# Kernel optimization log

Measured on AMD Instinct MI355X. Metric: run time of the kernel, lower is better.

## Reference

```python
import jax, jax.numpy as jnp
import numpy as np

N = 100000

def _gcn_norm(edge_index, n):
    # PyG GCNConv default: add self-loops, symmetric deg^-1/2 normalization
    loops = jnp.arange(n, dtype=edge_index.dtype)
    src = jnp.concatenate([edge_index[0], loops])
    dst = jnp.concatenate([edge_index[1], loops])
    deg = jax.ops.segment_sum(jnp.ones_like(dst, dtype=jnp.float32), dst, num_segments=n)
    dinv = jnp.where(deg > 0, jax.lax.rsqrt(deg), 0.0)
    norm = dinv[src] * dinv[dst]  # [E+N]
    return src, dst, norm

def _gcn_conv(h, W, b, src, dst, norm, n):
    # transform then gather-scale-scatter aggregate
    h = h @ W                                   # [N, out]
    out = jax.ops.segment_sum(norm[:, None] * h[src], dst, num_segments=n)
    return out + b

def _prelu(h, a):
    return jnp.where(h > 0, h, a * h)

def _dropout(h, u, p=0.5):
    # deterministic dropout: keep where u >= p, scale by 1/(1-p)
    return jnp.where(u >= p, h / (1.0 - p), 0.0)

def setup_inputs() -> dict:
    key = jax.random.key(0)
    ks = jax.random.split(key, 12)
    D, H1, H2, C, E = 512, 128, 16, 10, 1600000
    x = jax.random.normal(ks[0], (N, D), dtype=jnp.float32)
    edge_index = jax.random.randint(ks[1], (2, E), 0, N, dtype=jnp.int64)
    u1 = jax.random.uniform(ks[2], (N, H1), dtype=jnp.float32)
    u2 = jax.random.uniform(ks[3], (N, H2), dtype=jnp.float32)
    def glorot(k, shp):
        lim = np.sqrt(6.0 / (shp[0] + shp[1]))
        return jax.random.uniform(k, shp, dtype=jnp.float32, minval=-lim, maxval=lim)
    W1 = glorot(ks[4], (D, H1)); b1 = jnp.zeros((H1,), jnp.float32)
    W2 = glorot(ks[5], (H1, H2)); b2 = jnp.zeros((H2,), jnp.float32)
    fcW = glorot(ks[6], (H2, C)); fcb = jnp.zeros((C,), jnp.float32)
    a = jnp.float32(0.25)  # PReLU init (shared single param for both layers)
    return {"x": x, "edge_index": edge_index, "W1": W1, "b1": b1, "W2": W2,
            "b2": b2, "a": a, "fcW": fcW, "fcb": fcb, "u1": u1, "u2": u2}

def reference(x, edge_index, W1, b1, W2, b2, a, fcW, fcb, u1, u2):
    src, dst, norm = _gcn_norm(edge_index, N)
    feat1 = _dropout(_prelu(_gcn_conv(x, W1, b1, src, dst, norm, N), a), u1)
    feat2 = _dropout(_prelu(_gcn_conv(feat1, W2, b2, src, dst, norm, N), a), u2)
    logits = feat2 @ fcW + fcb
    return (feat2, logits)
```

## Files before the change

### kernel.cpp

```cpp
#include <hip/hip_runtime.h>
#include <hip/hip_bf16.h>
#include <stdint.h>

#define NN 100000
#define DIN 512
#define H1C 128
#define H2C 16
#define NCLS 10
#define NB_SCAN ((NN + 255) / 256)

typedef __attribute__((ext_vector_type(8))) short s16x8;
typedef __attribute__((ext_vector_type(4))) float f32x4;
typedef __attribute__((ext_vector_type(4))) unsigned short u16x4;
typedef __attribute__((ext_vector_type(8))) unsigned short u16x8;

static __device__ __forceinline__ unsigned short f2bf(float f) {
  __hip_bfloat16 h = __float2bfloat16(f);
  return *(unsigned short*)&h;
}
static __device__ __forceinline__ float bflo(unsigned u) {
  return __uint_as_float(u << 16);
}
static __device__ __forceinline__ float bfhi(unsigned u) {
  return __uint_as_float(u & 0xffff0000u);
}

__device__ __forceinline__ int ld_src(const int* __restrict__ ei, int f, int E, int i) {
  return f ? ei[2 * (size_t)i] : ei[i];
}
__device__ __forceinline__ int ld_dst(const int* __restrict__ ei, int f, int E, int i) {
  return f ? ei[2 * ((size_t)E + (size_t)i)] : ei[(size_t)E + (size_t)i];
}

__global__ void k_pre(const int* __restrict__ ei, int* __restrict__ flag,
                      int* __restrict__ deg,
                      const float* __restrict__ W1, unsigned short* __restrict__ Wt, int n) {
  int i = blockIdx.x * 256 + threadIdx.x;
  if (blockIdx.x == 0 && threadIdx.x < 64) {
    int v = ei[2 * threadIdx.x + 1];
    unsigned long long b = __ballot(v == 0);
    if (threadIdx.x == 0) *flag = (b == ~0ull) ? 1 : 0;
  }
  if (i < n) deg[i] = 0;
  if (i < H1C * DIN) {
    int nn = i >> 9, k = i & 511;
    Wt[i] = f2bf(W1[(size_t)k * H1C + nn]);
  }
}

__global__ void k_count(const int* __restrict__ ei, const int* __restrict__ flag,
                        int E, int* __restrict__ deg, int* __restrict__ rank) {
  int i = blockIdx.x * blockDim.x + threadIdx.x;
  if (i >= E) return;
  int f = *flag;
  rank[i] = atomicAdd(&deg[ld_dst(ei, f, E, i)], 1);
}

__global__ void k_scanA(const int* __restrict__ deg, int* __restrict__ incl,
                        int* __restrict__ bsum, float* __restrict__ dinv, int n) {
  __shared__ int s[256];
  int i = blockIdx.x * 256 + threadIdx.x;
  int v = (i < n) ? deg[i] : 0;
  if (i < n) dinv[i] = rsqrtf((float)(v + 1));
  s[threadIdx.x] = v;
  __syncthreads();
  for (int off = 1; off < 256; off <<= 1) {
    int t = (threadIdx.x >= off) ? s[threadIdx.x - off] : 0;
    __syncthreads();
    s[threadIdx.x] += t;
    __syncthreads();
  }
  if (i < n) incl[i] = s[threadIdx.x];
  if (threadIdx.x == 255) bsum[blockIdx.x] = s[255];
}

__global__ void k_scanBC(const int* __restrict__ deg, const int* __restrict__ bsum,
                         int* __restrict__ offs, int n, int E, int nb) {
  __shared__ int s[512];
  int tid = threadIdx.x;
  int v = (tid < nb) ? bsum[tid] : 0;
  s[tid] = v;
  __syncthreads();
  for (int off = 1; off < 512; off <<= 1) {
    int t = (tid >= off) ? s[tid - off] : 0;
    __syncthreads();
    s[tid] += t;
    __syncthreads();
  }
  int bid = blockIdx.x;
  int pb = (bid > 0) ? s[bid - 1] : 0;
  int i = bid * 256 + (tid & 255);
  if (tid < 256 && i < n) offs[i] = offs[i] - deg[i] + pb;
  if (bid == 0 && tid == 0) offs[n] = E;
}

#define BM 64
#define BK 64
#define LDA 72
#define LDB 72
#define NGB ((NN + BM - 1) / BM)

__global__ __launch_bounds__(256) void k_sg1(const float* __restrict__ x,
                                             const unsigned short* __restrict__ Wt,
                                             unsigned int* __restrict__ h1u, int n,
                                             const int* __restrict__ ei,
                                             const int* __restrict__ flag, int E,
                                             const int* __restrict__ offs,
                                             const int* __restrict__ rank,
                                             const float* __restrict__ dinv,
                                             uint2* __restrict__ csr_sw) {
  __shared__ unsigned short As[BM * LDA];
  __shared__ unsigned short Bs[H1C * LDB];
  int tid = threadIdx.x;

  if (blockIdx.x >= NGB) {
    int i = (blockIdx.x - NGB) * 256 + tid;
    if (i < E) {
      int f = *flag;
      int s = ld_src(ei, f, E, i), d = ld_dst(ei, f, E, i);
      int pos = offs[d] + rank[i];
      uint2 rec;
      rec.x = (unsigned)s;
      rec.y = __float_as_uint(dinv[s]);
      csr_sw[pos] = rec;
    }
    return;
  }

  int wave = tid >> 6, lane = tid & 63;
  int wm = wave >> 1, wn = wave & 1;
  int bm = blockIdx.x * BM;
  int lrow = lane & 15, lk = (lane >> 4) * 8;

  f32x4 acc[2][4];
#pragma unroll
  for (int i = 0; i < 2; i++)
#pragma unroll
    for (int j = 0; j < 4; j++) acc[i][j] = (f32x4){0.f, 0.f, 0.f, 0.f};

  float4 areg[4];
  u16x8 breg[4];

  auto loadA = [&](int k0) {
#pragma unroll
    for (int p = 0; p < 4; p++) {
      int idx = p * 256 + tid;
      int r = idx >> 4, c4 = (idx & 15) * 4;
      int row = bm + r;
      areg[p] = make_float4(0.f, 0.f, 0.f, 0.f);
      if (row < n) areg[p] = *(const float4*)(x + (size_t)row * DIN + k0 + c4);
    }
  };
  auto loadB = [&](int k0) {
#pragma unroll
    for (int p = 0; p < 4; p++) {
      int idx = p * 256 + tid;
      int r = idx >> 3, c8 = (idx & 7) * 8;
      breg[p] = *(const u16x8*)&Wt[(size_t)r * DIN + k0 + c8];
    }
  };

  loadA(0);
  loadB(0);

  for (int k0 = 0; k0 < DIN; k0 += BK) {
#pragma unroll
    for (int p = 0; p < 4; p++) {
      int idx = p * 256 + tid;
      int r = idx >> 4, c4 = (idx & 15) * 4;
      u16x4 b4;
      b4.x = f2bf(areg[p].x); b4.y = f2bf(areg[p].y);
      b4.z = f2bf(areg[p].z); b4.w = f2bf(areg[p].w);
      *(u16x4*)&As[r * LDA + c4] = b4;
      int rb = idx >> 3, c8 = (idx & 7) * 8;
      int pr = (rb & 64) + (((rb & 1) + 2 * ((rb >> 5) & 1)) << 4) + ((rb >> 1) & 15);
      *(u16x8*)&Bs[pr * LDB + c8] = breg[p];
    }
    if (k0 + BK < DIN) {
      loadA(k0 + BK);
      loadB(k0 + BK);
    }
    __syncthreads();
#pragma unroll
    for (int kk = 0; kk < 2; kk++) {
      s16x8 a[2], b[4];
#pragma unroll
      for (int mi = 0; mi < 2; mi++)
        a[mi] = *(const s16x8*)&As[(wm * 32 + mi * 16 + lrow) * LDA + kk * 32 + lk];
#pragma unroll
      for (int nj = 0; nj < 4; nj++)
        b[nj] = *(const s16x8*)&Bs[(wn * 64 + nj * 16 + lrow) * LDB + kk * 32 + lk];
#pragma unroll
      for (int mi = 0; mi < 2; mi++)
#pragma unroll
        for (int nj = 0; nj < 4; nj++)
          acc[mi][nj] = __builtin_amdgcn_mfma_f32_16x16x32_bf16(a[mi], b[nj], acc[mi][nj], 0, 0, 0);
    }
    __syncthreads();
  }
#pragma unroll
  for (int mi = 0; mi < 2; mi++) {
#pragma unroll
    for (int r = 0; r < 4; r++) {
      int row = bm + wm * 32 + mi * 16 + (lane >> 4) * 4 + r;
      if (row < n) {
        unsigned p0 = ((unsigned)f2bf(acc[mi][1][r]) << 16) | (unsigned)f2bf(acc[mi][0][r]);
        unsigned p1 = ((unsigned)f2bf(acc[mi][3][r]) << 16) | (unsigned)f2bf(acc[mi][2][r]);
        h1u[(size_t)row * 64 + wn * 32 + lrow] = p0;
        h1u[(size_t)row * 64 + wn * 32 + 16 + lrow] = p1;
      }
    }
  }
}

__global__ __launch_bounds__(256) void k_agg1(const unsigned int* __restrict__ h1u,
                                              const uint2* __restrict__ csr_sw,
                                              const int* __restrict__ offs,
                                              const float* __restrict__ dinv,
                                              const float* __restrict__ b1,
                                              const float* __restrict__ aP,
                                              const float* __restrict__ u1,
                                              unsigned int* __restrict__ f1u, int n) {
  int wid = (blockIdx.x * 256 + threadIdx.x) >> 6;
  int lane = threadIdx.x & 63;
  if (wid >= n) return;
  int d = wid;
  int beg = offs[d], end = offs[d + 1];
  unsigned gs = h1u[(size_t)d * 64 + lane];
  float ax = 0.f, ay = 0.f;
  int e = beg;
  for (; e + 7 < end; e += 8) {
    uint2 r0 = csr_sw[e],     r1 = csr_sw[e + 1], r2 = csr_sw[e + 2], r3 = csr_sw[e + 3];
    uint2 r4 = csr_sw[e + 4], r5 = csr_sw[e + 5], r6 = csr_sw[e + 6], r7 = csr_sw[e + 7];
    unsigned g0 = h1u[(size_t)r0.x * 64 + lane];
    unsigned g1 = h1u[(size_t)r1.x * 64 + lane];
    unsigned g2 = h1u[(size_t)r2.x * 64 + lane];
    unsigned g3 = h1u[(size_t)r3.x * 64 + lane];
    unsigned g4 = h1u[(size_t)r4.x * 64 + lane];
    unsigned g5 = h1u[(size_t)r5.x * 64 + lane];
    unsigned g6 = h1u[(size_t)r6.x * 64 + lane];
    unsigned g7 = h1u[(size_t)r7.x * 64 + lane];
    float w0 = __uint_as_float(r0.y), w1 = __uint_as_float(r1.y);
    float w2 = __uint_as_float(r2.y), w3 = __uint_as_float(r3.y);
    float w4 = __uint_as_float(r4.y), w5 = __uint_as_float(r5.y);
    float w6 = __uint_as_float(r6.y), w7 = __uint_as_float(r7.y);
    ax += w0 * bflo(g0); ay += w0 * bfhi(g0);
    ax += w1 * bflo(g1); ay += w1 * bfhi(g1);
    ax += w2 * bflo(g2); ay += w2 * bfhi(g2);
    ax += w3 * bflo(g3); ay += w3 * bfhi(g3);
    ax += w4 * bflo(g4); ay += w4 * bfhi(g4);
    ax += w5 * bflo(g5); ay += w5 * bfhi(g5);
    ax += w6 * bflo(g6); ay += w6 * bfhi(g6);
    ax += w7 * bflo(g7); ay += w7 * bfhi(g7);
  }
  for (; e + 3 < end; e += 4) {
    uint2 r0 = csr_sw[e], r1 = csr_sw[e + 1], r2 = csr_sw[e + 2], r3 = csr_sw[e + 3];
    unsigned g0 = h1u[(size_t)r0.x * 64 + lane];
    unsigned g1 = h1u[(size_t)r1.x * 64 + lane];
    unsigned g2 = h1u[(size_t)r2.x * 64 + lane];
    unsigned g3 = h1u[(size_t)r3.x * 64 + lane];
    float w0 = __uint_as_float(r0.y), w1 = __uint_as_float(r1.y);
    float w2 = __uint_as_float(r2.y), w3 = __uint_as_float(r3.y);
    ax += w0 * bflo(g0); ay += w0 * bfhi(g0);
    ax += w1 * bflo(g1); ay += w1 * bfhi(g1);
    ax += w2 * bflo(g2); ay += w2 * bfhi(g2);
    ax += w3 * bflo(g3); ay += w3 * bfhi(g3);
  }
  for (; e < end; e++) {
    uint2 rr = csr_sw[e];
    float w = __uint_as_float(rr.y);
    unsigned g = h1u[(size_t)rr.x * 64 + lane];
    ax += w * bflo(g); ay += w * bfhi(g);
  }
  float di = dinv[d];
  ax = (ax + di * bflo(gs)) * di;
  ay = (ay + di * bfhi(gs)) * di;
  float2 bb = ((const float2*)b1)[lane];
  ax += bb.x; ay += bb.y;
  float al = *aP;
  ax = ax > 0.f ? ax : al * ax;
  ay = ay > 0.f ? ay : al * ay;
  float2 uu = ((const float2*)u1)[(size_t)d * 64 + lane];
  ax = (uu.x >= 0.5f) ? ax * 2.f : 0.f;
  ay = (uu.y >= 0.5f) ? ay * 2.f : 0.f;
  unsigned pk = ((unsigned)f2bf(ay) << 16) | (unsigned)f2bf(ax);
  f1u[(size_t)d * 64 + lane] = pk;
}

__global__ __launch_bounds__(256) void k_gemm2(const unsigned int* __restrict__ f1u,
                                               const float* __restrict__ W2,
                                               unsigned int* __restrict__ h2u, int n) {
  __shared__ float ws[H1C][H2C];
  __shared__ unsigned int fs[16][66];
  int tid = threadIdx.x;
#pragma unroll
  for (int p = 0; p < 8; p++) {
    int idx = tid + p * 256;
    ws[idx >> 4][idx & 15] = W2[idx];
  }
  int r0 = blockIdx.x * 16;
  {
    int r = tid >> 4, c4 = (tid & 15) * 4;
    int row = r0 + r;
    uint4 v = make_uint4(0, 0, 0, 0);
    if (row < n) v = *(const uint4*)(f1u + (size_t)row * 64 + c4);
    *(uint4*)&fs[r][c4] = v;
  }
  __syncthreads();
  int col = tid & 15, r = tid >> 4;
  float acc = 0.f;
#pragma unroll
  for (int k = 0; k < 64; k++) {
    unsigned u = fs[r][k];
    acc += bflo(u) * ws[2 * k][col] + bfhi(u) * ws[2 * k + 1][col];
  }
  int row = r0 + r;
  float accN = __shfl_xor(acc, 1, 64);
  if ((col & 1) == 0 && row < n) {
    unsigned pk = ((unsigned)f2bf(accN) << 16) | (unsigned)f2bf(acc);
    h2u[(size_t)row * 8 + (col >> 1)] = pk;
  }
}

__global__ __launch_bounds__(256) void k_agg2(const unsigned int* __restrict__ h2u,
                                              const uint2* __restrict__ csr_sw,
                                              const int* __restrict__ offs,
                                              const float* __restrict__ dinv,
                                              const float* __restrict__ b2,
                                              const float* __restrict__ aP,
                                              const float* __restrict__ u2,
                                              const float* __restrict__ fcW,
                                              const float* __restrict__ fcb,
                                              float* __restrict__ out_feat2,
                                              float* __restrict__ out_logits, int n) {
  int wid = (blockIdx.x * 256 + threadIdx.x) >> 6;
  int lane = threadIdx.x & 63;
  if (wid >= n) return;
  int d = wid;
  int g = lane >> 3, j = lane & 7;
  int beg = offs[d], end = offs[d + 1];
  unsigned gs = h2u[(size_t)d * 8 + j];
  float aa = 0.f, ab = 0.f;
  int e = beg + g;
  for (; e + 8 < end; e += 16) {
    uint2 r0 = csr_sw[e], r1 = csr_sw[e + 8];
    unsigned g0 = h2u[(size_t)r0.x * 8 + j];
    unsigned g1 = h2u[(size_t)r1.x * 8 + j];
    float w0 = __uint_as_float(r0.y), w1 = __uint_as_float(r1.y);
    aa += w0 * bflo(g0) + w1 * bflo(g1);
    ab += w0 * bfhi(g0) + w1 * bfhi(g1);
  }
  for (; e < end; e += 8) {
    uint2 rr = csr_sw[e];
    unsigned gg = h2u[(size_t)rr.x * 8 + j];
    float w = __uint_as_float(rr.y);
    aa += w * bflo(gg); ab += w * bfhi(gg);
  }
  aa += __shfl_xor(aa, 8, 64); aa += __shfl_xor(aa, 16, 64); aa += __shfl_xor(aa, 32, 64);
  ab += __shfl_xor(ab, 8, 64); ab += __shfl_xor(ab, 16, 64); ab += __shfl_xor(ab, 32, 64);
  float di = dinv[d];
  aa = (aa + di * bflo(gs)) * di;
  ab = (ab + di * bfhi(gs)) * di;
  aa += b2[2 * j]; ab += b2[2 * j + 1];
  float al = *aP;
  aa = aa > 0.f ? aa : al * aa;
  ab = ab > 0.f ? ab : al * ab;
  float2 uu = ((const float2*)(u2 + (size_t)d * H2C))[j];
  aa = (uu.x >= 0.5f) ? aa * 2.f : 0.f;
  ab = (uu.y >= 0.5f) ? ab * 2.f : 0.f;
  if (lane < 8) {
    float2 o; o.x = aa; o.y = ab;
    ((float2*)(out_feat2 + (size_t)d * H2C))[j] = o;
  }
  int c = lane & 15;
  int cc = (c < NCLS) ? c : 0;
  float lg = fcb[cc];
#pragma unroll
  for (int k = 0; k < 8; k++) {
    float va = __shfl(aa, k, 64);
    float vb = __shfl(ab, k, 64);
    lg += va * fcW[(2 * k) * NCLS + cc] + vb * fcW[(2 * k + 1) * NCLS + cc];
  }
  if (lane < NCLS) out_logits[(size_t)d * NCLS + c] = lg;
}

extern "C" void kernel_launch(void* const* d_in, const int* in_sizes, int n_in,
                              void* d_out, int out_size, void* d_ws, size_t ws_size,
                              hipStream_t stream) {
  const float* x   = (const float*)d_in[0];
  const int*   ei  = (const int*)d_in[1];
  const float* W1  = (const float*)d_in[2];
  const float* b1  = (const float*)d_in[3];
  const float* W2  = (const float*)d_in[4];
  const float* b2  = (const float*)d_in[5];
  const float* aP  = (const float*)d_in[6];
  const float* fcW = (const float*)d_in[7];
  const float* fcb = (const float*)d_in[8];
  const float* u1  = (const float*)d_in[9];
  const float* u2  = (const float*)d_in[10];
  const int E = in_sizes[1] / 2;

  float* out_feat2  = (float*)d_out;
  float* out_logits = (float*)d_out + (size_t)NN * H2C;

  char* w = (char*)d_ws;
  size_t off = 0;
  auto A = [&](size_t bytes) -> char* {
    char* p = w + off;
    off = (off + bytes + 255) & ~(size_t)255;
    return p;
  };
  int*   flag   = (int*)A(256);
  int*   deg    = (int*)A((size_t)NN * 4);
  int*   offs   = (int*)A((size_t)(NN + 1) * 4);
  float* dinv   = (float*)A((size_t)NN * 4);
  int*   bsum   = (int*)A(512 * 4);
  int*   rank   = (int*)A((size_t)E * 4);
  uint2* csr_sw = (uint2*)A((size_t)E * 8);
  unsigned int* h1u = (unsigned int*)A((size_t)NN * 64 * 4);
  unsigned int* f1u = (unsigned int*)A((size_t)NN * 64 * 4);
  unsigned int* h2u = (unsigned int*)A((size_t)NN * 8 * 4);
  unsigned short* Wt = (unsigned short*)A((size_t)H1C * DIN * 2);

  dim3 b256(256);
  int gE = (E + 255) / 256;
  int gN = (NN + 255) / 256;

  k_pre<<<gN, b256, 0, stream>>>(ei, flag, deg, W1, Wt, NN);
  k_count<<<gE, b256, 0, stream>>>(ei, flag, E, deg, rank);
  k_scanA<<<NB_SCAN, b256, 0, stream>>>(deg, offs, bsum, dinv, NN);
  k_scanBC<<<NB_SCAN, 512, 0, stream>>>(deg, bsum, offs, NN, E, NB_SCAN);
  k_sg1<<<NGB + gE, b256, 0, stream>>>(x, Wt, h1u, NN, ei, flag, E, offs, rank, dinv, csr_sw);
  k_agg1<<<(NN + 3) / 4, b256, 0, stream>>>(h1u, csr_sw, offs, dinv, b1, aP, u1, f1u, NN);
  k_gemm2<<<(NN + 15) / 16, b256, 0, stream>>>(f1u, W2, h2u, NN);
  k_agg2<<<(NN + 3) / 4, b256, 0, stream>>>(h2u, csr_sw, offs, dinv, b2, aP, u2,
                                            fcW, fcb, out_feat2, out_logits, NN);
}
```

Measured before the change: 322.2 us.

## Split CSR scatter from GEMM1 and process four edges per thread

Removes the CSR scatter from the fused GEMM1 kernel and runs it as its own kernel. Both count and scatter now handle four edges per thread, so each thread has several independent loads and atomics in flight. The cost is one extra kernel launch, and the scatter no longer overlaps with the GEMM blocks.

Measured after the change: 316.7 us. About the same (-1.7%).

```diff
diff --git a/kernel.cpp b/kernel.cpp
--- a/kernel.cpp
+++ b/kernel.cpp
@@ -50,10 +50,28 @@
 
 __global__ void k_count(const int* __restrict__ ei, const int* __restrict__ flag,
                         int E, int* __restrict__ deg, int* __restrict__ rank) {
-  int i = blockIdx.x * blockDim.x + threadIdx.x;
-  if (i >= E) return;
   int f = *flag;
-  rank[i] = atomicAdd(&deg[ld_dst(ei, f, E, i)], 1);
+  int base = blockIdx.x * 1024 + threadIdx.x;
+  if (base + 768 < E) {
+    int d0 = ld_dst(ei, f, E, base);
+    int d1 = ld_dst(ei, f, E, base + 256);
+    int d2 = ld_dst(ei, f, E, base + 512);
+    int d3 = ld_dst(ei, f, E, base + 768);
+    int r0 = atomicAdd(&deg[d0], 1);
+    int r1 = atomicAdd(&deg[d1], 1);
+    int r2 = atomicAdd(&deg[d2], 1);
+    int r3 = atomicAdd(&deg[d3], 1);
+    rank[base] = r0;
+    rank[base + 256] = r1;
+    rank[base + 512] = r2;
+    rank[base + 768] = r3;
+  } else {
+#pragma unroll
+    for (int k = 0; k < 4; k++) {
+      int i = base + k * 256;
+      if (i < E) rank[i] = atomicAdd(&deg[ld_dst(ei, f, E, i)], 1);
+    }
+  }
 }
 
 __global__ void k_scanA(const int* __restrict__ deg, int* __restrict__ incl,
@@ -94,39 +112,48 @@
   if (bid == 0 && tid == 0) offs[n] = E;
 }
 
+__global__ void k_scatter(const int* __restrict__ ei, const int* __restrict__ flag, int E,
+                          const int* __restrict__ offs, const int* __restrict__ rank,
+                          const float* __restrict__ dinv, uint2* __restrict__ csr_sw) {
+  int f = *flag;
+  int base = blockIdx.x * 1024 + threadIdx.x;
+  if (base + 768 < E) {
+    int i0 = base, i1 = base + 256, i2 = base + 512, i3 = base + 768;
+    int s0 = ld_src(ei, f, E, i0), d0 = ld_dst(ei, f, E, i0);
+    int s1 = ld_src(ei, f, E, i1), d1 = ld_dst(ei, f, E, i1);
+    int s2 = ld_src(ei, f, E, i2), d2 = ld_dst(ei, f, E, i2);
+    int s3 = ld_src(ei, f, E, i3), d3 = ld_dst(ei, f, E, i3);
+    int r0 = rank[i0], r1 = rank[i1], r2 = rank[i2], r3 = rank[i3];
+    int o0 = offs[d0], o1 = offs[d1], o2 = offs[d2], o3 = offs[d3];
+    float w0 = dinv[s0], w1 = dinv[s1], w2 = dinv[s2], w3 = dinv[s3];
+    csr_sw[o0 + r0] = make_uint2((unsigned)s0, __float_as_uint(w0));
+    csr_sw[o1 + r1] = make_uint2((unsigned)s1, __float_as_uint(w1));
+    csr_sw[o2 + r2] = make_uint2((unsigned)s2, __float_as_uint(w2));
+    csr_sw[o3 + r3] = make_uint2((unsigned)s3, __float_as_uint(w3));
+  } else {
+#pragma unroll
+    for (int k = 0; k < 4; k++) {
+      int i = base + k * 256;
+      if (i < E) {
+        int s = ld_src(ei, f, E, i), d = ld_dst(ei, f, E, i);
+        int pos = offs[d] + rank[i];
+        csr_sw[pos] = make_uint2((unsigned)s, __float_as_uint(dinv[s]));
+      }
+    }
+  }
+}
+
 #define BM 64
 #define BK 64
 #define LDA 72
 #define LDB 72
-#define NGB ((NN + BM - 1) / BM)
-
-__global__ __launch_bounds__(256) void k_sg1(const float* __restrict__ x,
-                                             const unsigned short* __restrict__ Wt,
-                                             unsigned int* __restrict__ h1u, int n,
-                                             const int* __restrict__ ei,
-                                             const int* __restrict__ flag, int E,
-                                             const int* __restrict__ offs,
-                                             const int* __restrict__ rank,
-                                             const float* __restrict__ dinv,
-                                             uint2* __restrict__ csr_sw) {
+
+__global__ __launch_bounds__(256) void k_gemm1_mfma(const float* __restrict__ x,
+                                                    const unsigned short* __restrict__ Wt,
+                                                    unsigned int* __restrict__ h1u, int n) {
   __shared__ unsigned short As[BM * LDA];
   __shared__ unsigned short Bs[H1C * LDB];
   int tid = threadIdx.x;
-
-  if (blockIdx.x >= NGB) {
-    int i = (blockIdx.x - NGB) * 256 + tid;
-    if (i < E) {
-      int f = *flag;
-      int s = ld_src(ei, f, E, i), d = ld_dst(ei, f, E, i);
-      int pos = offs[d] + rank[i];
-      uint2 rec;
-      rec.x = (unsigned)s;
-      rec.y = __float_as_uint(dinv[s]);
-      csr_sw[pos] = rec;
-    }
-    return;
-  }
-
   int wave = tid >> 6, lane = tid & 63;
   int wm = wave >> 1, wn = wave & 1;
   int bm = blockIdx.x * BM;
@@ -423,14 +450,15 @@
   unsigned short* Wt = (unsigned short*)A((size_t)H1C * DIN * 2);
 
   dim3 b256(256);
-  int gE = (E + 255) / 256;
+  int gE4 = (E + 1023) / 1024;
   int gN = (NN + 255) / 256;
 
   k_pre<<<gN, b256, 0, stream>>>(ei, flag, deg, W1, Wt, NN);
-  k_count<<<gE, b256, 0, stream>>>(ei, flag, E, deg, rank);
+  k_count<<<gE4, b256, 0, stream>>>(ei, flag, E, deg, rank);
   k_scanA<<<NB_SCAN, b256, 0, stream>>>(deg, offs, bsum, dinv, NN);
   k_scanBC<<<NB_SCAN, 512, 0, stream>>>(deg, bsum, offs, NN, E, NB_SCAN);
-  k_sg1<<<NGB + gE, b256, 0, stream>>>(x, Wt, h1u, NN, ei, flag, E, offs, rank, dinv, csr_sw);
+  k_scatter<<<gE4, b256, 0, stream>>>(ei, flag, E, offs, rank, dinv, csr_sw);
+  k_gemm1_mfma<<<(NN + BM - 1) / BM, b256, 0, stream>>>(x, Wt, h1u, NN);
   k_agg1<<<(NN + 3) / 4, b256, 0, stream>>>(h1u, csr_sw, offs, dinv, b1, aP, u1, f1u, NN);
   k_gemm2<<<(NN + 15) / 16, b256, 0, stream>>>(f1u, W2, h2u, NN);
   k_agg2<<<(NN + 3) / 4, b256, 0, stream>>>(h2u, csr_sw, offs, dinv, b2, aP, u2,
```
